# Optimization experiments

Measured on AMD Instinct MI355X. Metric: run time of the kernel, lower is better.

## Reference

```python
import jax, jax.numpy as jnp
import numpy as np

B, C, F_IN, F_OUT = 2048, 63, 250, 250
NEG_SLOPE = 0.2
N = B * C  # flattened node count


def _build_edge_index():
    # fixed fully-connected (no self) graph over the FIRST 63 nodes only
    src = np.array([i for i in range(C) for j in range(C) if i != j], dtype=np.int32)
    dst = np.array([j for i in range(C) for j in range(C) if i != j], dtype=np.int32)
    # PyG GATConv add_self_loops=True: self loop for every node (num_nodes = N)
    loops = np.arange(N, dtype=np.int32)
    src = np.concatenate([src, loops])
    dst = np.concatenate([dst, loops])
    return jnp.asarray(np.stack([src, dst]))  # [2, E]


def setup_inputs() -> dict:
    key = jax.random.key(0)
    kx, kw, ks, kd = jax.random.split(key, 4)
    x = jax.random.normal(kx, (B, 1, C, F_IN), dtype=jnp.float32)
    # GATConv params (heads=1): lin weight, att_src, att_dst, bias
    W = jax.random.normal(kw, (F_IN, F_OUT), dtype=jnp.float32) / np.sqrt(F_IN)
    att_src = jax.random.normal(ks, (F_OUT,), dtype=jnp.float32) / np.sqrt(F_OUT)
    att_dst = jax.random.normal(kd, (F_OUT,), dtype=jnp.float32) / np.sqrt(F_OUT)
    bias = jnp.zeros((F_OUT,), dtype=jnp.float32)
    return {"x": x, "W": W, "att_src": att_src, "att_dst": att_dst,
            "bias": bias, "edge_index": _build_edge_index()}


def reference(x, W, att_src, att_dst, bias, edge_index):
    b, _, c, f = x.shape
    n = b * c
    h = x.reshape(n, f) @ W                      # [N, F_OUT]
    a_src = h @ att_src                          # [N]
    a_dst = h @ att_dst                          # [N]
    src, dst = edge_index[0], edge_index[1]
    e = jax.nn.leaky_relu(a_src[src] + a_dst[dst], NEG_SLOPE)  # [E]
    # segment softmax over incoming edges of each dst node (stable)
    m = jax.ops.segment_max(e, dst, num_segments=n)
    ex = jnp.exp(e - m[dst])
    denom = jax.ops.segment_sum(ex, dst, num_segments=n)
    alpha = ex / denom[dst]                      # [E]
    out = jax.ops.segment_sum(alpha[:, None] * h[src], dst, num_segments=n)
    out = out + bias
    return out.reshape(b, 1, c, -1)              # [B,1,63,F_OUT]
```

## Files before the change

kernel.cpp:

```cpp
#include <hip/hip_runtime.h>
#include <cstdint>
#include <cstddef>

#define M_TOTAL 129024
#define KDIM    250
#define NDIM    250
#define BM      64
#define LASTR   264

typedef float  f32x4  __attribute__((ext_vector_type(4)));
typedef __bf16 bf16x8 __attribute__((ext_vector_type(8)));

static __device__ __forceinline__ unsigned short f2bf(float f) {
  unsigned u = __float_as_uint(f);
  u += 0x7fffu + ((u >> 16) & 1u);
  return (unsigned short)(u >> 16);
}

static __device__ __forceinline__ float wsum(float v) {
#pragma unroll
  for (int o = 32; o > 0; o >>= 1) v += __shfl_xor(v, o, 64);
  return v;
}
static __device__ __forceinline__ float wmaxr(float v) {
#pragma unroll
  for (int o = 32; o > 0; o >>= 1) v = fmaxf(v, __shfl_xor(v, o, 64));
  return v;
}

__global__ void wcvt_kernel(const float* __restrict__ W, unsigned short* __restrict__ WTf) {
  const int f     = blockIdx.x * 256 + threadIdx.x;
  const int lane  = f & 63;
  const int kk    = (f >> 6) & 7;
  const int ntile = f >> 9;
  const int n     = ntile * 16 + (lane & 15);
  const int k0    = kk * 32 + (lane >> 4) * 8;
  unsigned u[4];
#pragma unroll
  for (int p = 0; p < 4; ++p) {
    const int ka = k0 + 2 * p, kb = k0 + 2 * p + 1;
    unsigned short a = (n < NDIM && ka < KDIM) ? f2bf(W[(size_t)ka * NDIM + n]) : 0;
    unsigned short b = (n < NDIM && kb < KDIM) ? f2bf(W[(size_t)kb * NDIM + n]) : 0;
    u[p] = (unsigned)a | ((unsigned)b << 16);
  }
  *reinterpret_cast<uint4*>(WTf + (size_t)f * 8) = make_uint4(u[0], u[1], u[2], u[3]);
}

__global__ __launch_bounds__(256, 2) void gemm_kernel(
    const float* __restrict__ X, const unsigned short* __restrict__ WTf,
    const float* __restrict__ bias, float* __restrict__ out,
    float* __restrict__ h63) {
  __shared__ unsigned short lA[BM * LASTR];

  const int mBase = blockIdx.x * BM;
  const int tid  = threadIdx.x;
  const int lane = tid & 63;
  const int w    = tid >> 6;
  const int r16  = lane & 15;
  const int quad = lane >> 4;

  const float* Xs = X + (size_t)mBase * KDIM;

  float2 av[32];
#pragma unroll
  for (int j = 0; j < 32; ++j) {
    const int idx = j * 256 + tid;
    if (j < 31 || tid < 64)
      av[j] = *reinterpret_cast<const float2*>(Xs + (size_t)idx * 2);
  }

  bf16x8 bfrag[4][8];
#pragma unroll
  for (int nt = 0; nt < 4; ++nt)
#pragma unroll
    for (int kk = 0; kk < 8; ++kk)
      bfrag[nt][kk] = *reinterpret_cast<const bf16x8*>(
          WTf + (size_t)((((w * 4 + nt) * 8) + kk) * 64 + lane) * 8);

#pragma unroll
  for (int j = 0; j < 32; ++j) {
    const int idx = j * 256 + tid;
    if (j < 31 || tid < 64) {
      const int r = idx / 125;
      const int c = idx - r * 125;
      const unsigned p = (unsigned)f2bf(av[j].x) | ((unsigned)f2bf(av[j].y) << 16);
      *reinterpret_cast<unsigned*>(&lA[r * LASTR + c * 2]) = p;
    }
  }
  if (tid < 64) {
#pragma unroll
    for (int c = 250; c < 264; c += 2)
      *reinterpret_cast<unsigned*>(&lA[tid * LASTR + c]) = 0u;
  }
  __syncthreads();

  f32x4 acc[4][4];
#pragma unroll
  for (int mt = 0; mt < 4; ++mt)
#pragma unroll
    for (int nt = 0; nt < 4; ++nt)
      acc[mt][nt] = f32x4{0.f, 0.f, 0.f, 0.f};

#pragma unroll
  for (int kk = 0; kk < 8; ++kk) {
    bf16x8 aF[4];
#pragma unroll
    for (int mt = 0; mt < 4; ++mt)
      aF[mt] = *reinterpret_cast<const bf16x8*>(
          &lA[(mt * 16 + r16) * LASTR + kk * 32 + quad * 8]);
#pragma unroll
    for (int mt = 0; mt < 4; ++mt)
#pragma unroll
      for (int nt = 0; nt < 4; ++nt)
        acc[mt][nt] = __builtin_amdgcn_mfma_f32_16x16x32_bf16(aF[mt], bfrag[nt][kk],
                                                              acc[mt][nt], 0, 0, 0);
  }

#pragma unroll
  for (int nt = 0; nt < 4; ++nt) {
    const int col = w * 64 + nt * 16 + r16;
    if (col < NDIM) {
      const float bv = bias[col];
#pragma unroll
      for (int mt = 0; mt < 4; ++mt) {
        const int rb = mBase + mt * 16 + quad * 4;
        f32x4 a = acc[mt][nt];
#pragma unroll
        for (int i = 0; i < 4; ++i)
          out[(size_t)(rb + i) * NDIM + col] = a[i] + bv;
      }
    }
  }
  if (mBase == 0) {
#pragma unroll
    for (int nt = 0; nt < 4; ++nt) {
      const int col = w * 64 + nt * 16 + r16;
      if (col < NDIM) {
#pragma unroll
        for (int mt = 0; mt < 4; ++mt) {
          const int rb = mt * 16 + quad * 4;
          f32x4 a = acc[mt][nt];
#pragma unroll
          for (int i = 0; i < 4; ++i)
            if (rb + i < 63) h63[(rb + i) * NDIM + col] = a[i];
        }
      }
    }
  }
}

__global__ void att_kernel(const float* __restrict__ h, const float* __restrict__ att_src,
                           const float* __restrict__ att_dst, const float* __restrict__ bias,
                           float* __restrict__ out) {
  const int d = blockIdx.x;
  const int tid = threadIdx.x;
  const int lane = tid & 63;
  const int wid = tid >> 6;

  __shared__ float s_asrc[64];
  __shared__ float s_adst;
  __shared__ float s_alpha[64];

  for (int s = wid; s < 63; s += 4) {
    float sum = 0.f;
    for (int f = lane; f < NDIM; f += 64) sum += h[s * NDIM + f] * att_src[f];
    sum = wsum(sum);
    if (lane == 0) s_asrc[s] = sum;
  }
  if (wid == 0) {
    float sum = 0.f;
    for (int f = lane; f < NDIM; f += 64) sum += h[d * NDIM + f] * att_dst[f];
    sum = wsum(sum);
    if (lane == 0) s_adst = sum;
  }
  __syncthreads();

  if (wid == 0) {
    float e = -__builtin_inff();
    if (lane < 63) {
      float x = s_asrc[lane] + s_adst;
      e = (x > 0.f) ? x : 0.2f * x;
    }
    const float m = wmaxr(e);
    const float p = (lane < 63) ? expf(e - m) : 0.f;
    const float den = wsum(p);
    s_alpha[lane] = p / den;
  }
  __syncthreads();

  const int f = tid;
  if (f < NDIM) {
    float o = bias[f];
    for (int s = 0; s < 63; ++s) o += s_alpha[s] * h[s * NDIM + f];
    out[(size_t)d * NDIM + f] = o;
  }
}

extern "C" void kernel_launch(void* const* d_in, const int* in_sizes, int n_in,
                              void* d_out, int out_size, void* d_ws, size_t ws_size,
                              hipStream_t stream) {
  const float* X       = (const float*)d_in[0];
  const float* W       = (const float*)d_in[1];
  const float* att_src = (const float*)d_in[2];
  const float* att_dst = (const float*)d_in[3];
  const float* bias    = (const float*)d_in[4];
  float* out = (float*)d_out;

  unsigned short* WTf = (unsigned short*)d_ws;
  float* h63 = (float*)((char*)d_ws + 131072);

  wcvt_kernel<<<32, 256, 0, stream>>>(W, WTf);
  gemm_kernel<<<M_TOTAL / BM, 256, 0, stream>>>(X, WTf, bias, out, h63);
  att_kernel<<<63, 256, 0, stream>>>(h63, att_src, att_dst, bias, out);
}
```

Before: 287.2 us.

## Stream fp32 X tiles directly into LDS and convert to bf16 at fragment load

Replaces the register-staged global load plus bf16 conversion and padded LDS store with direct global-to-LDS async copies of the raw fp32 X slab. The bf16 conversion moves into the MFMA fragment load using add-and-permute (round-half-up rather than round-to-nearest-even). This removes register pressure and a conversion pass before the barrier. In exchange, LDS use doubles to about 64KB per block and fragment reads become fp32 with unpadded row stride, which may cause bank conflicts.

```diff
diff --git a/kernel.cpp b/kernel.cpp
--- a/kernel.cpp
+++ b/kernel.cpp
@@ -6,7 +6,7 @@
 #define KDIM    250
 #define NDIM    250
 #define BM      64
-#define LASTR   264
+#define LDSB    64032
 
 typedef float  f32x4  __attribute__((ext_vector_type(4)));
 typedef __bf16 bf16x8 __attribute__((ext_vector_type(8)));
@@ -50,7 +50,8 @@
     const float* __restrict__ X, const unsigned short* __restrict__ WTf,
     const float* __restrict__ bias, float* __restrict__ out,
     float* __restrict__ h63) {
-  __shared__ unsigned short lA[BM * LASTR];
+  __shared__ uint4 lA4[LDSB / 16];
+  unsigned char* lA = (unsigned char*)lA4;
 
   const int mBase = blockIdx.x * BM;
   const int tid  = threadIdx.x;
@@ -59,15 +60,24 @@
   const int r16  = lane & 15;
   const int quad = lane >> 4;
 
-  const float* Xs = X + (size_t)mBase * KDIM;
-
-  float2 av[32];
-#pragma unroll
-  for (int j = 0; j < 32; ++j) {
-    const int idx = j * 256 + tid;
-    if (j < 31 || tid < 64)
-      av[j] = *reinterpret_cast<const float2*>(Xs + (size_t)idx * 2);
-  }
+  {
+    const char* slab = (const char*)X + (size_t)mBase * (KDIM * 4);
+#pragma unroll
+    for (int i = 0; i < 16; ++i) {
+      const int blk = i * 4 + w;
+      if (blk < 62) {
+        __builtin_amdgcn_global_load_lds(
+            (__attribute__((address_space(1))) void*)(slab + blk * 1024 + lane * 16),
+            (__attribute__((address_space(3))) void*)(lA + blk * 1024), 16, 0, 0);
+      }
+    }
+    if (w == 3 && lane < 32) {
+      __builtin_amdgcn_global_load_lds(
+          (__attribute__((address_space(1))) void*)(slab + 63488 + lane * 16),
+          (__attribute__((address_space(3))) void*)(lA + 63488), 16, 0, 0);
+    }
+  }
+  if (tid < 8) *reinterpret_cast<unsigned*>(lA + 64000 + tid * 4) = 0u;
 
   bf16x8 bfrag[4][8];
 #pragma unroll
@@ -77,21 +87,6 @@
       bfrag[nt][kk] = *reinterpret_cast<const bf16x8*>(
           WTf + (size_t)((((w * 4 + nt) * 8) + kk) * 64 + lane) * 8);
 
-#pragma unroll
-  for (int j = 0; j < 32; ++j) {
-    const int idx = j * 256 + tid;
-    if (j < 31 || tid < 64) {
-      const int r = idx / 125;
-      const int c = idx - r * 125;
-      const unsigned p = (unsigned)f2bf(av[j].x) | ((unsigned)f2bf(av[j].y) << 16);
-      *reinterpret_cast<unsigned*>(&lA[r * LASTR + c * 2]) = p;
-    }
-  }
-  if (tid < 64) {
-#pragma unroll
-    for (int c = 250; c < 264; c += 2)
-      *reinterpret_cast<unsigned*>(&lA[tid * LASTR + c]) = 0u;
-  }
   __syncthreads();
 
   f32x4 acc[4][4];
@@ -101,13 +96,23 @@
     for (int nt = 0; nt < 4; ++nt)
       acc[mt][nt] = f32x4{0.f, 0.f, 0.f, 0.f};
 
+  const float* lAf = (const float*)lA;
 #pragma unroll
   for (int kk = 0; kk < 8; ++kk) {
     bf16x8 aF[4];
 #pragma unroll
-    for (int mt = 0; mt < 4; ++mt)
-      aF[mt] = *reinterpret_cast<const bf16x8*>(
-          &lA[(mt * 16 + r16) * LASTR + kk * 32 + quad * 8]);
+    for (int mt = 0; mt < 4; ++mt) {
+      const int r = mt * 16 + r16;
+      const int c = kk * 32 + quad * 8;
+      const uint2* p = reinterpret_cast<const uint2*>(lAf + r * KDIM + c);
+      uint2 q0 = p[0], q1 = p[1], q2 = p[2], q3 = p[3];
+      uint4 P;
+      P.x = __builtin_amdgcn_perm(q0.y + 0x8000u, q0.x + 0x8000u, 0x07060302u);
+      P.y = __builtin_amdgcn_perm(q1.y + 0x8000u, q1.x + 0x8000u, 0x07060302u);
+      P.z = __builtin_amdgcn_perm(q2.y + 0x8000u, q2.x + 0x8000u, 0x07060302u);
+      P.w = __builtin_amdgcn_perm(q3.y + 0x8000u, q3.x + 0x8000u, 0x07060302u);
+      aF[mt] = __builtin_bit_cast(bf16x8, P);
+    }
 #pragma unroll
     for (int mt = 0; mt < 4; ++mt)
 #pragma unroll
```

Result: no change. 291.6 us (+1.5%).
